# Kernel tuning notes

Measured on AMD Instinct MI355X. Metric: run time of the kernel, lower is better.

The kernel has to match this reference:

```python
import jax, jax.numpy as jnp
import numpy as np

HIDDEN = 1024
HEADS = 16
HEAD = HIDDEN // HEADS
B, S = 2, 2048


def setup_inputs() -> dict:
    key = jax.random.key(0)
    ks = jax.random.split(key, 8)
    query = jax.random.normal(ks[0], (B, S, HIDDEN), dtype=jnp.float32)
    key_t = jax.random.normal(ks[1], (B, S, HIDDEN), dtype=jnp.float32)
    value = jax.random.normal(ks[2], (B, S, HIDDEN), dtype=jnp.float32)
    # causal mask, broadcastable over batch and heads; 0 -> masked (-inf)
    mask = jnp.tril(jnp.ones((S, S), dtype=jnp.int32))[None, None, :, :]
    # torch Linear weights are [out_features, in_features]
    scale = 0.02
    Wq = jax.random.normal(ks[3], (HIDDEN, HIDDEN), dtype=jnp.float32) * scale
    Wk = jax.random.normal(ks[4], (HIDDEN, HIDDEN), dtype=jnp.float32) * scale
    Wv = jax.random.normal(ks[5], (HIDDEN, HIDDEN), dtype=jnp.float32) * scale
    Wo = jax.random.normal(ks[6], (HIDDEN, HIDDEN), dtype=jnp.float32) * scale
    bo = jax.random.normal(ks[7], (HIDDEN,), dtype=jnp.float32) * scale
    return {"query": query, "key": key_t, "value": value, "mask": mask,
            "Wq": Wq, "Wk": Wk, "Wv": Wv, "Wo": Wo, "bo": bo}


def reference(query, key, value, mask, Wq, Wk, Wv, Wo, bo):
    b = query.shape[0]
    # Linear (no bias): x @ W^T, then split into heads -> [b, h, s, d]
    def heads(x, W):
        y = jnp.einsum('bse,oe->bso', x, W)
        return y.reshape(b, -1, HEADS, HEAD).transpose(0, 2, 1, 3)
    Q = heads(query, Wq)
    K = heads(key, Wk)
    V = heads(value, Wv)
    inv_scale = 1.0 / jnp.sqrt(jnp.float32(HEAD))
    scores = jnp.einsum('bhqd,bhkd->bhqk', Q, K) * inv_scale  # [b,h,s,s]
    scores = jnp.where(mask == 0, -jnp.inf, scores)
    attn = jax.nn.softmax(scores, axis=-1)
    x = jnp.einsum('bhqk,bhkd->bhqd', attn, V)
    x = x.transpose(0, 2, 1, 3).reshape(b, -1, HIDDEN)
    return jnp.einsum('bse,oe->bso', x, Wo) + bo
```

## Files before the change

### kernel.cpp

```cpp
#include <hip/hip_runtime.h>


typedef __attribute__((ext_vector_type(8))) short short8;
typedef __attribute__((ext_vector_type(4))) float f32x4;
typedef unsigned int u32;
typedef unsigned short u16;

__device__ inline f32x4 mfma16(short8 a, short8 b, f32x4 c) {
    return __builtin_amdgcn_mfma_f32_16x16x32_bf16(a, b, c, 0, 0, 0);
}
__device__ inline u16 f2bf(float f) {
    union { float f; u32 u; } v; v.f = f;
    u32 r = v.u + 0x7fff + ((v.u >> 16) & 1);
    return (u16)(r >> 16);
}
__device__ inline void gll16(void* lds, const void* g) {
    __builtin_amdgcn_global_load_lds((const __attribute__((address_space(1))) u32*)g,
                                     (__attribute__((address_space(3))) u32*)lds,
                                     16, 0, 0);
}
__device__ inline u32 pkbf(float hi, float lo) {
    return __builtin_amdgcn_perm(__float_as_uint(hi), __float_as_uint(lo),
                                 0x07060302u);
}

__global__ __launch_bounds__(256)
void cvt_all(const float* __restrict__ q, const float* __restrict__ k,
             const float* __restrict__ v, const float* __restrict__ wq,
             const float* __restrict__ wk, const float* __restrict__ wv,
             const float* __restrict__ wo,
             u16* __restrict__ q16, u16* __restrict__ k16,
             u16* __restrict__ v16, u16* __restrict__ w16) {
    const size_t QKV = 1u << 22;
    const size_t WSZ = 1u << 20;
    size_t base = ((size_t)blockIdx.x * 256 + threadIdx.x) * 8;
    const float* src; u16* dst; size_t off; float scale = 1.0f;
    if (base < QKV)            { src = q; dst = q16; off = base;
                                 scale = 0.125f * 1.44269504f; }
    else if (base < 2 * QKV)   { src = k; dst = k16; off = base - QKV;     }
    else if (base < 3 * QKV)   { src = v; dst = v16; off = base - 2 * QKV; }
    else {
        size_t wb = base - 3 * QKV;
        int wi = (int)(wb >> 20); off = wb & (WSZ - 1);
        src = wi == 0 ? wq : wi == 1 ? wk : wi == 2 ? wv : wo;
        dst = w16 + (size_t)wi * WSZ;
    }
    float4 f0 = *(const float4*)(src + off);
    float4 f1 = *(const float4*)(src + off + 4);
    short8 s = { (short)f2bf(f0.x * scale), (short)f2bf(f0.y * scale),
                 (short)f2bf(f0.z * scale), (short)f2bf(f0.w * scale),
                 (short)f2bf(f1.x * scale), (short)f2bf(f1.y * scale),
                 (short)f2bf(f1.z * scale), (short)f2bf(f1.w * scale) };
    *(short8*)(dst + off) = s;
}

__global__ __launch_bounds__(256)
void gemm_qkv(const u16* __restrict__ q16, const u16* __restrict__ k16,
              const u16* __restrict__ v16, const u16* __restrict__ w16,
              u16* __restrict__ Qg, u16* __restrict__ Kg, u16* __restrict__ Vt) {
    const int K = 1024;
    __shared__ u16 As[3][128 * 32];
    __shared__ u16 Bs[3][128 * 32];
    const int z = blockIdx.z;
    const u16* A = z == 0 ? q16 : z == 1 ? k16 : v16;
    const u16* W = w16 + (size_t)z * (1u << 20);

    const int tid = threadIdx.x, lane = tid & 63, w = tid >> 6;
    const int ln15 = lane & 15, quad = lane >> 4;
    const int fr = (ln15 >> 1) & 3;
    const int lrow = lane >> 2;
    const int lcs = (((lane & 3) ^ ((lane >> 3) & 3)) << 3);
    const int m0 = blockIdx.y * 128, n0 = blockIdx.x * 128;
    const int wm = (w >> 1) * 64, wn = (w & 1) * 64;

    f32x4 acc[4][4] = {};

    #pragma unroll
    for (int t = 0; t < 2; ++t)
        #pragma unroll
        for (int c = 0; c < 2; ++c) {
            gll16(&As[t][(w * 32 + c * 16) * 32],
                  &A[(size_t)(m0 + w * 32 + c * 16 + lrow) * K + t * 32 + lcs]);
            gll16(&Bs[t][(w * 32 + c * 16) * 32],
                  &W[(size_t)(n0 + w * 32 + c * 16 + lrow) * K + t * 32 + lcs]);
        }

    int cur = 0;
    for (int t = 0; t < 32; ++t) {
        if (t < 31) {
            __asm__ volatile("s_waitcnt vmcnt(4)" ::: "memory");
        } else {
            __asm__ volatile("s_waitcnt vmcnt(0)" ::: "memory");
        }
        __builtin_amdgcn_s_barrier();
        __builtin_amdgcn_sched_barrier(0);

        if (t < 30) {
            const int k0 = (t + 2) * 32;
            const int nb = (cur + 2 >= 3) ? cur - 1 : cur + 2;
            #pragma unroll
            for (int c = 0; c < 2; ++c) {
                gll16(&As[nb][(w * 32 + c * 16) * 32],
                      &A[(size_t)(m0 + w * 32 + c * 16 + lrow) * K + k0 + lcs]);
                gll16(&Bs[nb][(w * 32 + c * 16) * 32],
                      &W[(size_t)(n0 + w * 32 + c * 16 + lrow) * K + k0 + lcs]);
            }
        }
        __builtin_amdgcn_sched_barrier(0);

        short8 a[4], b[4];
        #pragma unroll
        for (int mt = 0; mt < 4; ++mt)
            a[mt] = *(const short8*)&As[cur][(wm + mt * 16 + ln15) * 32 +
                                            ((quad ^ fr) << 3)];
        #pragma unroll
        for (int nt = 0; nt < 4; ++nt)
            b[nt] = *(const short8*)&Bs[cur][(wn + nt * 16 + ln15) * 32 +
                                            ((quad ^ fr) << 3)];
        #pragma unroll
        for (int mt = 0; mt < 4; ++mt)
            #pragma unroll
            for (int nt = 0; nt < 4; ++nt)
                acc[mt][nt] = mfma16(a[mt], b[nt], acc[mt][nt]);

        cur = (cur == 2) ? 0 : cur + 1;
    }

    #pragma unroll
    for (int mt = 0; mt < 4; ++mt)
        #pragma unroll
        for (int nt = 0; nt < 4; ++nt)
            #pragma unroll
            for (int r = 0; r < 4; ++r) {
                int m = m0 + wm + mt * 16 + quad * 4 + r;
                int n = n0 + wn + nt * 16 + ln15;
                u16 hv = f2bf(acc[mt][nt][r]);
                if (z == 2) {
                    int b_ = m >> 11, s_ = m & 2047, h_ = n >> 6, d_ = n & 63;
                    int kl = s_ & 63;
                    int sp = (s_ & ~63) + (kl & 15) * 4 + (kl >> 4);
                    Vt[((size_t)(b_ * 16 + h_) * 64 + d_) * 2048 + sp] = hv;
                } else {
                    u16* dst = z ? Kg : Qg;
                    dst[(size_t)m * 1024 + n] = hv;
                }
            }
}

__global__ __launch_bounds__(256)
void gemm_out(const u16* __restrict__ A, const u16* __restrict__ W,
              const float* __restrict__ bias, float* __restrict__ out) {
    const int K = 1024;
    __shared__ u16 As[3][64 * 64];
    __shared__ u16 Bs[3][128 * 64];
    const int id = blockIdx.x;
    const int by = id >> 3, bx = id & 7;

    const int tid = threadIdx.x, lane = tid & 63, w = tid >> 6;
    const int ln15 = lane & 15, quad = lane >> 4, s7 = ln15 & 7;
    const int lr = lane >> 3;
    const int lcs = (((lane & 7) ^ lr) << 3);
    const int m0 = by * 64, n0 = bx * 128;
    const int wm = (w & 1) * 32, wn = (w >> 1) * 64;

    f32x4 acc[2][4] = {};

    #pragma unroll
    for (int t = 0; t < 2; ++t) {
        #pragma unroll
        for (int c = 0; c < 2; ++c)
            gll16(&As[t][(w * 16 + c * 8) * 64],
                  &A[(size_t)(m0 + w * 16 + c * 8 + lr) * K + t * 64 + lcs]);
        #pragma unroll
        for (int c = 0; c < 4; ++c)
            gll16(&Bs[t][(w * 32 + c * 8) * 64],
                  &W[(size_t)(n0 + w * 32 + c * 8 + lr) * K + t * 64 + lcs]);
    }

    int cur = 0;
    for (int i = 0; i < 16; ++i) {
        if (i < 15) {
            __asm__ volatile("s_waitcnt vmcnt(6)" ::: "memory");
        } else {
            __asm__ volatile("s_waitcnt vmcnt(0)" ::: "memory");
        }
        __builtin_amdgcn_s_barrier();
        __builtin_amdgcn_sched_barrier(0);

        if (i < 14) {
            const int k0 = (i + 2) * 64;
            const int nb = (cur + 2 >= 3) ? cur - 1 : cur + 2;
            #pragma unroll
            for (int c = 0; c < 2; ++c)
                gll16(&As[nb][(w * 16 + c * 8) * 64],
                      &A[(size_t)(m0 + w * 16 + c * 8 + lr) * K + k0 + lcs]);
            #pragma unroll
            for (int c = 0; c < 4; ++c)
                gll16(&Bs[nb][(w * 32 + c * 8) * 64],
                      &W[(size_t)(n0 + w * 32 + c * 8 + lr) * K + k0 + lcs]);
        }
        __builtin_amdgcn_sched_barrier(0);

        #pragma unroll
        for (int kh = 0; kh < 2; ++kh) {
            short8 a[2], b[4];
            #pragma unroll
            for (int mt = 0; mt < 2; ++mt)
                a[mt] = *(const short8*)&As[cur][(wm + mt * 16 + ln15) * 64 +
                                                (((kh * 4 + quad) ^ s7) << 3)];
            #pragma unroll
            for (int nt = 0; nt < 4; ++nt)
                b[nt] = *(const short8*)&Bs[cur][(wn + nt * 16 + ln15) * 64 +
                                                (((kh * 4 + quad) ^ s7) << 3)];
            #pragma unroll
            for (int mt = 0; mt < 2; ++mt)
                #pragma unroll
                for (int nt = 0; nt < 4; ++nt)
                    acc[mt][nt] = mfma16(a[mt], b[nt], acc[mt][nt]);
        }
        cur = (cur == 2) ? 0 : cur + 1;
    }

    #pragma unroll
    for (int mt = 0; mt < 2; ++mt)
        #pragma unroll
        for (int nt = 0; nt < 4; ++nt)
            #pragma unroll
            for (int r = 0; r < 4; ++r) {
                int m = m0 + wm + mt * 16 + quad * 4 + r;
                int n = n0 + wn + nt * 16 + ln15;
                out[(size_t)m * 1024 + n] = acc[mt][nt][r] + bias[n];
            }
}

__global__ __launch_bounds__(256)
void attn3(const u16* __restrict__ Qg, const u16* __restrict__ Kg,
           const u16* __restrict__ Vt, u16* __restrict__ Xb) {
    __shared__ u16 Kl[2][64 * 64];
    __shared__ u16 Vl[2][64 * 64];
    __shared__ u16 Pl[4][16 * 64];

    const int id = blockIdx.x;
    const int bh = id & 31, qt = 31 - (id >> 5);
    const int b = bh >> 4, h = bh & 15;
    const int tid = threadIdx.x, lane = tid & 63, w = tid >> 6;
    const int ln15 = lane & 15, quad = lane >> 4, s7 = ln15 & 7;
    const int lr = lane >> 3;
    const int lcs = (((lane & 7) ^ lr) << 3);
    const u16* Kbase = Kg + (size_t)b * 2048 * 1024 + h * 64;
    const u16* Vbase = Vt + (size_t)bh * 64 * 2048;
    const float M0L = 8.65617025f;
    const int q0 = qt * 64;

    const u16* qrow = Qg + (size_t)(b * 2048 + q0 + w * 16 + ln15) * 1024 + h * 64;
    short8 aq0 = *(const short8*)(qrow + quad * 8);
    short8 aq1 = *(const short8*)(qrow + 32 + quad * 8);
    __asm__ volatile("s_waitcnt vmcnt(0)" ::: "memory");

    f32x4 o[4] = {};
    float lsum[4] = {0.f, 0.f, 0.f, 0.f};

    #pragma unroll
    for (int c = 0; c < 2; ++c) {
        const int r0 = w * 16 + c * 8;
        gll16(&Kl[0][r0 * 64], Kbase + (size_t)(r0 + lr) * 1024 + lcs);
        gll16(&Vl[0][r0 * 64], Vbase + (size_t)(r0 + lr) * 2048 + lcs);
    }

    for (int kt = 0; kt <= qt; ++kt) {
        const int cur = kt & 1, nb = cur ^ 1;
        __asm__ volatile("s_waitcnt vmcnt(0)" ::: "memory");
        __builtin_amdgcn_s_barrier();
        __builtin_amdgcn_sched_barrier(0);

        if (kt < qt) {
            const int nk = (kt + 1) * 64;
            #pragma unroll
            for (int c = 0; c < 2; ++c) {
                const int r0 = w * 16 + c * 8;
                gll16(&Kl[nb][r0 * 64], Kbase + (size_t)(nk + r0 + lr) * 1024 + lcs);
                gll16(&Vl[nb][r0 * 64], Vbase + (size_t)(r0 + lr) * 2048 + nk + lcs);
            }
        }
        __builtin_amdgcn_sched_barrier(0);

        f32x4 sc[4];
        #pragma unroll
        for (int ct = 0; ct < 4; ++ct) {
            short8 b0 = *(const short8*)&Kl[cur][(ct * 16 + ln15) * 64 +
                                                ((quad ^ s7) << 3)];
            short8 b1 = *(const short8*)&Kl[cur][(ct * 16 + ln15) * 64 +
                                                (((4 + quad) ^ s7) << 3)];
            f32x4 c = {};
            c = mfma16(aq0, b0, c);
            c = mfma16(aq1, b1, c);
            sc[ct] = c;
        }

        const bool diag = (kt == qt);
        #pragma unroll
        for (int r = 0; r < 4; ++r) {
            float s0 = sc[0][r], s1 = sc[1][r], s2 = sc[2][r], s3 = sc[3][r];
            if (diag) {
                const int qq = w * 16 + quad * 4 + r;
                s0 = (ln15      <= qq) ? s0 : -1e30f;
                s1 = (16 + ln15 <= qq) ? s1 : -1e30f;
                s2 = (32 + ln15 <= qq) ? s2 : -1e30f;
                s3 = (48 + ln15 <= qq) ? s3 : -1e30f;
            }
            float p0 = __builtin_amdgcn_exp2f(s0 - M0L);
            float p1 = __builtin_amdgcn_exp2f(s1 - M0L);
            float p2 = __builtin_amdgcn_exp2f(s2 - M0L);
            float p3 = __builtin_amdgcn_exp2f(s3 - M0L);
            uint2 pw = make_uint2(pkbf(p1, p0), pkbf(p3, p2));
            *(uint2*)&Pl[w][(quad * 4 + r) * 64 + ln15 * 4] = pw;
            lsum[r] += (p0 + p1) + (p2 + p3);
        }

        __asm__ volatile("s_waitcnt lgkmcnt(0)" ::: "memory");
        short8 ap0 = *(const short8*)&Pl[w][ln15 * 64 + quad * 8];
        short8 ap1 = *(const short8*)&Pl[w][ln15 * 64 + 32 + quad * 8];

        #pragma unroll
        for (int dt = 0; dt < 4; ++dt) {
            short8 bv0 = *(const short8*)&Vl[cur][(dt * 16 + ln15) * 64 +
                                                 ((quad ^ s7) << 3)];
            short8 bv1 = *(const short8*)&Vl[cur][(dt * 16 + ln15) * 64 +
                                                 (((4 + quad) ^ s7) << 3)];
            o[dt] = mfma16(ap0, bv0, o[dt]);
            o[dt] = mfma16(ap1, bv1, o[dt]);
        }
    }

    #pragma unroll
    for (int r = 0; r < 4; ++r) {
        float l = lsum[r];
        #pragma unroll
        for (int off = 1; off < 16; off <<= 1)
            l += __shfl_xor(l, off);
        lsum[r] = l;
    }
    #pragma unroll
    for (int dt = 0; dt < 4; ++dt)
        #pragma unroll
        for (int r = 0; r < 4; ++r) {
            int q = q0 + w * 16 + quad * 4 + r;
            Xb[(size_t)(b * 2048 + q) * 1024 + h * 64 + dt * 16 + ln15] =
                f2bf(o[dt][r] / lsum[r]);
        }
}

extern "C" void kernel_launch(void* const* d_in, const int* in_sizes, int n_in,
                              void* d_out, int out_size, void* d_ws, size_t ws_size,
                              hipStream_t stream) {
    const float* query = (const float*)d_in[0];
    const float* key   = (const float*)d_in[1];
    const float* value = (const float*)d_in[2];
    const float* Wq = (const float*)d_in[4];
    const float* Wk = (const float*)d_in[5];
    const float* Wv = (const float*)d_in[6];
    const float* Wo = (const float*)d_in[7];
    const float* bo = (const float*)d_in[8];
    float* out = (float*)d_out;

    u16* ws  = (u16*)d_ws;
    const size_t T = 1ull << 22;
    u16* q16 = ws;
    u16* k16 = ws + T;
    u16* v16 = ws + 2 * T;
    u16* w16 = ws + 3 * T;
    u16* Qg  = ws + 4 * T;
    u16* Kg  = ws + 5 * T;
    u16* Vt  = (u16*)d_out;
    u16* Xb  = q16;
    const size_t WSZ = 1ull << 20;

    cvt_all<<<8192, 256, 0, stream>>>(query, key, value, Wq, Wk, Wv, Wo,
                                      q16, k16, v16, w16);

    gemm_qkv<<<dim3(8, 32, 3), 256, 0, stream>>>(q16, k16, v16, w16, Qg, Kg, Vt);

    attn3<<<1024, 256, 0, stream>>>(Qg, Kg, Vt, Xb);

    gemm_out<<<512, 256, 0, stream>>>(Xb, w16 + 3 * WSZ, bo, out);
}
```

Before: 221.5 us.

## Fuse activation fp32-to-bf16 conversion into QKV GEMM loads

Stops pre-converting query/key/value to bf16 in a separate pass. The QKV GEMM now loads fp32 tiles straight into LDS and converts them, with the Q scale applied, while building MFMA operands. This removes a full read/write pass over the three activation tensors. In exchange it doubles the A-tile LDS footprint, drops from a triple-buffered to a double-buffered pipeline with a full vmcnt(0) wait every step, and adds conversion ALU work to the inner loop, which is repeated across the 8 N-tile blocks.

Result: slower. 235.4 us (+6.3%).

```diff
diff --git a/kernel.cpp b/kernel.cpp
--- a/kernel.cpp
+++ b/kernel.cpp
@@ -14,6 +14,11 @@
     u32 r = v.u + 0x7fff + ((v.u >> 16) & 1);
     return (u16)(r >> 16);
 }
+__device__ inline u32 pk2bf(float lo, float hi) {
+    u32 ul = __float_as_uint(lo); ul += 0x7fff + ((ul >> 16) & 1);
+    u32 uh = __float_as_uint(hi); uh += 0x7fff + ((uh >> 16) & 1);
+    return __builtin_amdgcn_perm(uh, ul, 0x07060302u);
+}
 __device__ inline void gll16(void* lds, const void* g) {
     __builtin_amdgcn_global_load_lds((const __attribute__((address_space(1))) u32*)g,
                                      (__attribute__((address_space(3))) u32*)lds,
@@ -25,105 +30,98 @@
 }
 
 __global__ __launch_bounds__(256)
-void cvt_all(const float* __restrict__ q, const float* __restrict__ k,
-             const float* __restrict__ v, const float* __restrict__ wq,
-             const float* __restrict__ wk, const float* __restrict__ wv,
-             const float* __restrict__ wo,
-             u16* __restrict__ q16, u16* __restrict__ k16,
-             u16* __restrict__ v16, u16* __restrict__ w16) {
-    const size_t QKV = 1u << 22;
+void cvt_w(const float* __restrict__ wq, const float* __restrict__ wk,
+           const float* __restrict__ wv, const float* __restrict__ wo,
+           u16* __restrict__ w16) {
     const size_t WSZ = 1u << 20;
     size_t base = ((size_t)blockIdx.x * 256 + threadIdx.x) * 8;
-    const float* src; u16* dst; size_t off; float scale = 1.0f;
-    if (base < QKV)            { src = q; dst = q16; off = base;
-                                 scale = 0.125f * 1.44269504f; }
-    else if (base < 2 * QKV)   { src = k; dst = k16; off = base - QKV;     }
-    else if (base < 3 * QKV)   { src = v; dst = v16; off = base - 2 * QKV; }
-    else {
-        size_t wb = base - 3 * QKV;
-        int wi = (int)(wb >> 20); off = wb & (WSZ - 1);
-        src = wi == 0 ? wq : wi == 1 ? wk : wi == 2 ? wv : wo;
-        dst = w16 + (size_t)wi * WSZ;
-    }
+    int wi = (int)(base >> 20); size_t off = base & (WSZ - 1);
+    const float* src = wi == 0 ? wq : wi == 1 ? wk : wi == 2 ? wv : wo;
     float4 f0 = *(const float4*)(src + off);
     float4 f1 = *(const float4*)(src + off + 4);
-    short8 s = { (short)f2bf(f0.x * scale), (short)f2bf(f0.y * scale),
-                 (short)f2bf(f0.z * scale), (short)f2bf(f0.w * scale),
-                 (short)f2bf(f1.x * scale), (short)f2bf(f1.y * scale),
-                 (short)f2bf(f1.z * scale), (short)f2bf(f1.w * scale) };
-    *(short8*)(dst + off) = s;
+    short8 s = { (short)f2bf(f0.x), (short)f2bf(f0.y),
+                 (short)f2bf(f0.z), (short)f2bf(f0.w),
+                 (short)f2bf(f1.x), (short)f2bf(f1.y),
+                 (short)f2bf(f1.z), (short)f2bf(f1.w) };
+    *(short8*)(w16 + (size_t)wi * WSZ + off) = s;
 }
 
 __global__ __launch_bounds__(256)
-void gemm_qkv(const u16* __restrict__ q16, const u16* __restrict__ k16,
-              const u16* __restrict__ v16, const u16* __restrict__ w16,
+void gemm_qkv(const float* __restrict__ qf, const float* __restrict__ kf,
+              const float* __restrict__ vf, const u16* __restrict__ w16,
               u16* __restrict__ Qg, u16* __restrict__ Kg, u16* __restrict__ Vt) {
     const int K = 1024;
-    __shared__ u16 As[3][128 * 32];
-    __shared__ u16 Bs[3][128 * 32];
+    __shared__ float Af[2][128 * 32];
+    __shared__ u16  Bs[2][128 * 32];
     const int z = blockIdx.z;
-    const u16* A = z == 0 ? q16 : z == 1 ? k16 : v16;
+    const float* A = z == 0 ? qf : z == 1 ? kf : vf;
     const u16* W = w16 + (size_t)z * (1u << 20);
+    const float zscale = (z == 0) ? 0.125f * 1.44269504f : 1.0f;
 
     const int tid = threadIdx.x, lane = tid & 63, w = tid >> 6;
     const int ln15 = lane & 15, quad = lane >> 4;
-    const int fr = (ln15 >> 1) & 3;
-    const int lrow = lane >> 2;
-    const int lcs = (((lane & 3) ^ ((lane >> 3) & 3)) << 3);
+    const int frB  = (ln15 >> 1) & 3;
+    const int lrowB = lane >> 2;
+    const int lcsB = (((lane & 3) ^ ((lane >> 3) & 3)) << 3);
+    const int lrowA = lane >> 3;
+    const int lcsA = (((lane & 7) ^ ((lane >> 3) & 7)) << 2);
     const int m0 = blockIdx.y * 128, n0 = blockIdx.x * 128;
     const int wm = (w >> 1) * 64, wn = (w & 1) * 64;
 
     f32x4 acc[4][4] = {};
 
     #pragma unroll
-    for (int t = 0; t < 2; ++t)
-        #pragma unroll
-        for (int c = 0; c < 2; ++c) {
-            gll16(&As[t][(w * 32 + c * 16) * 32],
-                  &A[(size_t)(m0 + w * 32 + c * 16 + lrow) * K + t * 32 + lcs]);
-            gll16(&Bs[t][(w * 32 + c * 16) * 32],
-                  &W[(size_t)(n0 + w * 32 + c * 16 + lrow) * K + t * 32 + lcs]);
-        }
-
-    int cur = 0;
+    for (int c = 0; c < 4; ++c)
+        gll16(&Af[0][(w * 32 + c * 8) * 32],
+              &A[(size_t)(m0 + w * 32 + c * 8 + lrowA) * K + lcsA]);
+    #pragma unroll
+    for (int c = 0; c < 2; ++c)
+        gll16(&Bs[0][(w * 32 + c * 16) * 32],
+              &W[(size_t)(n0 + w * 32 + c * 16 + lrowB) * K + lcsB]);
+
     for (int t = 0; t < 32; ++t) {
+        const int cur = t & 1, nb = cur ^ 1;
+        __asm__ volatile("s_waitcnt vmcnt(0)" ::: "memory");
+        __builtin_amdgcn_s_barrier();
+        __builtin_amdgcn_sched_barrier(0);
+
         if (t < 31) {
-            __asm__ volatile("s_waitcnt vmcnt(4)" ::: "memory");
-        } else {
-            __asm__ volatile("s_waitcnt vmcnt(0)" ::: "memory");
-        }
-        __builtin_amdgcn_s_barrier();
-        __builtin_amdgcn_sched_barrier(0);
-
-        if (t < 30) {
-            const int k0 = (t + 2) * 32;
-            const int nb = (cur + 2 >= 3) ? cur - 1 : cur + 2;
-            #pragma unroll
-            for (int c = 0; c < 2; ++c) {
-                gll16(&As[nb][(w * 32 + c * 16) * 32],
-                      &A[(size_t)(m0 + w * 32 + c * 16 + lrow) * K + k0 + lcs]);
+            const int k0 = (t + 1) * 32;
+            #pragma unroll
+            for (int c = 0; c < 4; ++c)
+                gll16(&Af[nb][(w * 32 + c * 8) * 32],
+                      &A[(size_t)(m0 + w * 32 + c * 8 + lrowA) * K + k0 + lcsA]);
+            #pragma unroll
+            for (int c = 0; c < 2; ++c)
                 gll16(&Bs[nb][(w * 32 + c * 16) * 32],
-                      &W[(size_t)(n0 + w * 32 + c * 16 + lrow) * K + k0 + lcs]);
-            }
+                      &W[(size_t)(n0 + w * 32 + c * 16 + lrowB) * K + k0 + lcsB]);
         }
         __builtin_amdgcn_sched_barrier(0);
 
         short8 a[4], b[4];
         #pragma unroll
-        for (int mt = 0; mt < 4; ++mt)
-            a[mt] = *(const short8*)&As[cur][(wm + mt * 16 + ln15) * 32 +
-                                            ((quad ^ fr) << 3)];
+        for (int mt = 0; mt < 4; ++mt) {
+            const int R = wm + mt * 16 + ln15;
+            const int p0 = (2 * quad) ^ (R & 7);
+            const int p1 = p0 ^ 1;
+            f32x4 fa = *(const f32x4*)&Af[cur][R * 32 + (p0 << 2)];
+            f32x4 fb = *(const f32x4*)&Af[cur][R * 32 + (p1 << 2)];
+            union { u32 u[4]; short8 s; } au;
+            au.u[0] = pk2bf(fa[0] * zscale, fa[1] * zscale);
+            au.u[1] = pk2bf(fa[2] * zscale, fa[3] * zscale);
+            au.u[2] = pk2bf(fb[0] * zscale, fb[1] * zscale);
+            au.u[3] = pk2bf(fb[2] * zscale, fb[3] * zscale);
+            a[mt] = au.s;
+        }
         #pragma unroll
         for (int nt = 0; nt < 4; ++nt)
             b[nt] = *(const short8*)&Bs[cur][(wn + nt * 16 + ln15) * 32 +
-                                            ((quad ^ fr) << 3)];
+                                            ((quad ^ frB) << 3)];
         #pragma unroll
         for (int mt = 0; mt < 4; ++mt)
             #pragma unroll
             for (int nt = 0; nt < 4; ++nt)
                 acc[mt][nt] = mfma16(a[mt], b[nt], acc[mt][nt]);
-
-        cur = (cur == 2) ? 0 : cur + 1;
     }
 
     #pragma unroll
@@ -365,20 +363,17 @@
 
     u16* ws  = (u16*)d_ws;
     const size_t T = 1ull << 22;
-    u16* q16 = ws;
-    u16* k16 = ws + T;
-    u16* v16 = ws + 2 * T;
     u16* w16 = ws + 3 * T;
     u16* Qg  = ws + 4 * T;
     u16* Kg  = ws + 5 * T;
     u16* Vt  = (u16*)d_out;
-    u16* Xb  = q16;
+    u16* Xb  = ws;
     const size_t WSZ = 1ull << 20;
 
-    cvt_all<<<8192, 256, 0, stream>>>(query, key, value, Wq, Wk, Wv, Wo,
-                                      q16, k16, v16, w16);
-
-    gemm_qkv<<<dim3(8, 32, 3), 256, 0, stream>>>(q16, k16, v16, w16, Qg, Kg, Vt);
+    cvt_w<<<2048, 256, 0, stream>>>(Wq, Wk, Wv, Wo, w16);
+
+    gemm_qkv<<<dim3(8, 32, 3), 256, 0, stream>>>(query, key, value, w16,
+                                                 Qg, Kg, Vt);
 
     attn3<<<1024, 256, 0, stream>>>(Qg, Kg, Vt, Xb);
 
```
